# Performance work log

Measured on AMD Instinct MI355X. Metric: run time of the kernel, lower is better.

## Reference

```python
import jax, jax.numpy as jnp
import numpy as np

T, B, I, H = 512, 64, 1024, 1024
FORGET_BIAS = 1.0


def setup_inputs() -> dict:
    key = jax.random.key(0)
    ks = jax.random.split(key, 5)
    s = 0.02
    return {
        "x": jax.random.normal(ks[0], (T, B, I), dtype=jnp.float32),
        "Wx0": jax.random.normal(ks[1], (4 * H, I), dtype=jnp.float32) * s,
        "Wh0": jax.random.normal(ks[2], (4 * H, H), dtype=jnp.float32) * s,
        "Wx1": jax.random.normal(ks[3], (4 * H, H), dtype=jnp.float32) * s,
        "Wh1": jax.random.normal(ks[4], (4 * H, H), dtype=jnp.float32) * s,
    }


def _cell(x_t, h, c, Wx, Wh):
    # ifgo: [B, 4H]; gate chunk order in source is i, j, f, o
    ifgo = x_t @ Wx.T + h @ Wh.T
    i, j, f, o = jnp.split(ifgo, 4, axis=-1)
    c_next = c * jax.nn.sigmoid(f + FORGET_BIAS) + jax.nn.sigmoid(i) * jnp.tanh(j)
    h_next = jax.nn.sigmoid(o) * jnp.tanh(c_next)
    return h_next, c_next


def reference(x, Wx0, Wh0, Wx1, Wh1):
    b, hdim = x.shape[1], Wh0.shape[1]
    z = jnp.zeros((b, hdim), dtype=x.dtype)

    def step(carry, x_t):
        h0, c0, h1, c1 = carry
        h0, c0 = _cell(x_t, h0, c0, Wx0, Wh0)
        h1, c1 = _cell(h0, h1, c1, Wx1, Wh1)
        return (h0, c0, h1, c1), h1

    (h0, c0, h1, c1), out = jax.lax.scan(step, (z, z, z, z), x)
    h = jnp.stack([h0, h1])  # [n_layers, B, H]
    c = jnp.stack([c0, c1])
    return out, h, c
```

## Files before the change

### kernel.cpp

```cpp
#include <hip/hip_runtime.h>


#define T_STEPS 512
#define BATCH   64
#define HDIM    1024
#define KTOT    2048
#define BK      128
#define NITER   (KTOT / BK)
#define LDSTR   136
#define BH      (BATCH * HDIM)

typedef __bf16 bf16x8 __attribute__((ext_vector_type(8)));
typedef __bf16 bf16x4 __attribute__((ext_vector_type(4)));
typedef float  f32x4  __attribute__((ext_vector_type(4)));

__device__ __forceinline__ float sigm_(float x) { return 1.0f / (1.0f + __expf(-x)); }
__device__ __forceinline__ float tanh_(float x) {
    float e = __expf(-2.0f * fabsf(x));
    float t = (1.0f - e) / (1.0f + e);
    return copysignf(t, x);
}

__global__ __launch_bounds__(256) void lstm_step2(
    const __bf16* __restrict__ Ax0, const __bf16* __restrict__ Ah0,
    const __bf16* __restrict__ W0,  float* __restrict__ c0,
    __bf16* __restrict__ hb0, float* __restrict__ hf0, int en0,
    const __bf16* __restrict__ Ax1, const __bf16* __restrict__ Ah1,
    const __bf16* __restrict__ W1,  float* __restrict__ c1,
    __bf16* __restrict__ hb1, float* __restrict__ hf1, int en1)
{
    __shared__ __bf16 As[64 * LDSTR];
    __shared__ __bf16 Bs[64 * LDSTR];

    int bid = blockIdx.x;
    const __bf16 *Ax, *Ah, *W;
    float *c, *hf;
    __bf16 *hb;
    if (bid < 64) {
        if (!en0) return;
        Ax = Ax0; Ah = Ah0; W = W0; c = c0; hb = hb0; hf = hf0;
    } else {
        if (!en1) return;
        Ax = Ax1; Ah = Ah1; W = W1; c = c1; hb = hb1; hf = hf1; bid -= 64;
    }
    const int n0   = bid * 16;
    const int tid  = threadIdx.x;
    const int wave = tid >> 6;
    const int lane = tid & 63;
    const int sr   = tid >> 2;
    const int kc   = (tid & 3) * 32;
    const int wrow = (sr >> 4) * 1024 + n0 + (sr & 15);

    f32x4 acc[4] = {};

    bf16x8 pa[4], pb[4];
    {
        const __bf16* s = Ax + sr * 1024 + kc;
        #pragma unroll
        for (int u = 0; u < 4; ++u) pa[u] = *(const bf16x8*)(s + u * 8);
        const __bf16* w = W + wrow * 2048 + kc;
        #pragma unroll
        for (int u = 0; u < 4; ++u) pb[u] = *(const bf16x8*)(w + u * 8);
    }

    for (int it = 0; it < NITER; ++it) {
        #pragma unroll
        for (int u = 0; u < 4; ++u) *(bf16x8*)&As[sr * LDSTR + kc + u * 8] = pa[u];
        #pragma unroll
        for (int u = 0; u < 4; ++u) *(bf16x8*)&Bs[sr * LDSTR + kc + u * 8] = pb[u];
        __syncthreads();

        if (it + 1 < NITER) {
            int kb = (it + 1) * BK;
            const __bf16* s = (kb < 1024 ? Ax + sr * 1024 + kb
                                         : Ah + sr * 1024 + (kb - 1024)) + kc;
            #pragma unroll
            for (int u = 0; u < 4; ++u) pa[u] = *(const bf16x8*)(s + u * 8);
            const __bf16* w = W + wrow * 2048 + kb + kc;
            #pragma unroll
            for (int u = 0; u < 4; ++u) pb[u] = *(const bf16x8*)(w + u * 8);
        }

        const int lrow = lane & 15;
        const int lk   = (lane >> 4) * 8;
        #pragma unroll
        for (int s4 = 0; s4 < 4; ++s4) {
            bf16x8 af = *(bf16x8*)&As[(wave * 16 + lrow) * LDSTR + s4 * 32 + lk];
            #pragma unroll
            for (int g = 0; g < 4; ++g) {
                bf16x8 bf = *(bf16x8*)&Bs[(g * 16 + lrow) * LDSTR + s4 * 32 + lk];
                acc[g] = __builtin_amdgcn_mfma_f32_16x16x32_bf16(af, bf, acc[g], 0, 0, 0);
            }
        }
        __syncthreads();
    }

    const int n  = n0 + (lane & 15);
    const int mb = wave * 16 + (lane >> 4) * 4;
    #pragma unroll
    for (int r = 0; r < 4; ++r) {
        int m = mb + r;
        float gi = acc[0][r], gj = acc[1][r], gf = acc[2][r], go = acc[3][r];
        float cold = c[m * HDIM + n];
        float cn = cold * sigm_(gf + 1.0f) + sigm_(gi) * tanh_(gj);
        float hn = sigm_(go) * tanh_(cn);
        c[m * HDIM + n]  = cn;
        hb[m * HDIM + n] = (__bf16)hn;
        hf[m * HDIM + n] = hn;
    }
}

__global__ void convW(const float* __restrict__ Wx, const float* __restrict__ Wh,
                      __bf16* __restrict__ dst) {
    int i = blockIdx.x * 256 + threadIdx.x;
    int e = i * 4;
    int n = e >> 11;
    int k = e & 2047;
    const float* src = (k < 1024) ? (Wx + n * 1024 + k) : (Wh + n * 1024 + (k - 1024));
    float4 v = *(const float4*)src;
    bf16x4 o = { (__bf16)v.x, (__bf16)v.y, (__bf16)v.z, (__bf16)v.w };
    *(bf16x4*)(dst + e) = o;
}

__global__ void convX(const float* __restrict__ x, __bf16* __restrict__ dst) {
    int i = blockIdx.x * 256 + threadIdx.x;
    int e = i * 4;
    float4 v = *(const float4*)(x + e);
    bf16x4 o = { (__bf16)v.x, (__bf16)v.y, (__bf16)v.z, (__bf16)v.w };
    *(bf16x4*)(dst + e) = o;
}

__global__ void initz(__bf16* h0s, __bf16* h1s, float* c0, float* c1) {
    int i = blockIdx.x * 256 + threadIdx.x;
    h0s[i] = (__bf16)0.0f;
    h1s[i] = (__bf16)0.0f;
    c0[i] = 0.0f;
    c1[i] = 0.0f;
}

__global__ void epilogue_k(float* __restrict__ out, const float* __restrict__ h0f,
                           const float* __restrict__ c0, const float* __restrict__ c1) {
    int i = blockIdx.x * 256 + threadIdx.x;
    float* hout = out + (size_t)T_STEPS * BH;
    hout[i]      = h0f[i];
    hout[BH + i] = out[(size_t)(T_STEPS - 1) * BH + i];
    float* cout = hout + 2 * BH;
    cout[i]      = c0[i];
    cout[BH + i] = c1[i];
}

extern "C" void kernel_launch(void* const* d_in, const int* in_sizes, int n_in,
                              void* d_out, int out_size, void* d_ws, size_t ws_size,
                              hipStream_t stream) {
    const float* x   = (const float*)d_in[0];
    const float* Wx0 = (const float*)d_in[1];
    const float* Wh0 = (const float*)d_in[2];
    const float* Wx1 = (const float*)d_in[3];
    const float* Wh1 = (const float*)d_in[4];
    float* out = (float*)d_out;

    char* p = (char*)d_ws;
    __bf16* W0c = (__bf16*)p; p += (size_t)4096 * 2048 * 2;
    __bf16* W1c = (__bf16*)p; p += (size_t)4096 * 2048 * 2;
    __bf16* Xb  = (__bf16*)p; p += (size_t)T_STEPS * BH * 2;
    __bf16* h0s = (__bf16*)p; p += (size_t)2 * BH * 2;
    __bf16* h1s = (__bf16*)p; p += (size_t)2 * BH * 2;
    float*  c0v = (float*)p;  p += (size_t)BH * 4;
    float*  c1v = (float*)p;  p += (size_t)BH * 4;
    float*  h0f = (float*)p;  p += (size_t)BH * 4;

    convW<<<8192, 256, 0, stream>>>(Wx0, Wh0, W0c);
    convW<<<8192, 256, 0, stream>>>(Wx1, Wh1, W1c);
    convX<<<32768, 256, 0, stream>>>(x, Xb);
    initz<<<256, 256, 0, stream>>>(h0s, h1s, c0v, c1v);

    for (int s = 0; s <= T_STEPS; ++s) {
        int en0 = (s < T_STEPS);
        int en1 = (s >= 1);
        int t1  = en1 ? (s - 1) : 0;
        const __bf16* Ax0 = Xb + (size_t)(en0 ? s : 0) * BH;
        const __bf16* Ah0 = h0s + (size_t)(s & 1) * BH;
        __bf16*       hb0 = h0s + (size_t)((s & 1) ^ 1) * BH;
        const __bf16* Ax1 = h0s + (size_t)(s & 1) * BH;
        const __bf16* Ah1 = h1s + (size_t)(t1 & 1) * BH;
        __bf16*       hb1 = h1s + (size_t)((t1 & 1) ^ 1) * BH;
        float*        o1  = out + (size_t)t1 * BH;
        lstm_step2<<<128, 256, 0, stream>>>(Ax0, Ah0, W0c, c0v, hb0, h0f, en0,
                                            Ax1, Ah1, W1c, c1v, hb1, o1, en1);
    }

    epilogue_k<<<256, 256, 0, stream>>>(out, h0f, c0v, c1v);
}
```

Before: 10.50 ms.

## Replace per-step launches with persistent kernel holding weights in LDS

Measured after the change: 13.09 ms. 1.25x slower.

```diff
diff --git a/kernel.cpp b/kernel.cpp
--- a/kernel.cpp
+++ b/kernel.cpp
@@ -4,11 +4,8 @@
 #define T_STEPS 512
 #define BATCH   64
 #define HDIM    1024
-#define KTOT    2048
-#define BK      128
-#define NITER   (KTOT / BK)
-#define LDSTR   136
 #define BH      (BATCH * HDIM)
+#define LDS_BYTES (32 * 4096)
 
 typedef __bf16 bf16x8 __attribute__((ext_vector_type(8)));
 typedef __bf16 bf16x4 __attribute__((ext_vector_type(4)));
@@ -21,92 +18,127 @@
     return copysignf(t, x);
 }
 
-__global__ __launch_bounds__(256) void lstm_step2(
-    const __bf16* __restrict__ Ax0, const __bf16* __restrict__ Ah0,
-    const __bf16* __restrict__ W0,  float* __restrict__ c0,
-    __bf16* __restrict__ hb0, float* __restrict__ hf0, int en0,
-    const __bf16* __restrict__ Ax1, const __bf16* __restrict__ Ah1,
-    const __bf16* __restrict__ W1,  float* __restrict__ c1,
-    __bf16* __restrict__ hb1, float* __restrict__ hf1, int en1)
+__global__ __launch_bounds__(256, 1) void lstm_persist(
+    const __bf16* __restrict__ Xb,
+    const __bf16* __restrict__ W0, const __bf16* __restrict__ W1,
+    __bf16* __restrict__ h0s, __bf16* __restrict__ h1s,
+    float* __restrict__ out, float* __restrict__ h0f,
+    float* __restrict__ c0v, float* __restrict__ c1v,
+    int* __restrict__ flags)
 {
-    __shared__ __bf16 As[64 * LDSTR];
-    __shared__ __bf16 Bs[64 * LDSTR];
-
-    int bid = blockIdx.x;
-    const __bf16 *Ax, *Ah, *W;
-    float *c, *hf;
-    __bf16 *hb;
-    if (bid < 64) {
-        if (!en0) return;
-        Ax = Ax0; Ah = Ah0; W = W0; c = c0; hb = hb0; hf = hf0;
-    } else {
-        if (!en1) return;
-        Ax = Ax1; Ah = Ah1; W = W1; c = c1; hb = hb1; hf = hf1; bid -= 64;
+    extern __shared__ char smem[];
+    const int bid   = blockIdx.x;
+    const int tid   = threadIdx.x;
+    const int layer = bid >> 7;
+    const int cb    = bid & 127;
+    const int n0    = cb * 8;
+    const __bf16* W = layer ? W1 : W0;
+
+    for (int idx = tid; idx < 32 * 256; idx += 256) {
+        int lr = idx >> 8, ch = idx & 255;
+        int wrow = (lr >> 3) * 1024 + n0 + (lr & 7);
+        bf16x8 v = *(const bf16x8*)(W + (size_t)wrow * 2048 + ch * 8);
+        int db = lr * 4096 + ((ch * 16) ^ ((lr & 7) << 4));
+        *(bf16x8*)(smem + db) = v;
     }
-    const int n0   = bid * 16;
-    const int tid  = threadIdx.x;
+    __syncthreads();
+
+    const int lane = tid & 63;
     const int wave = tid >> 6;
-    const int lane = tid & 63;
-    const int sr   = tid >> 2;
-    const int kc   = (tid & 3) * 32;
-    const int wrow = (sr >> 4) * 1024 + n0 + (sr & 15);
-
-    f32x4 acc[4] = {};
-
-    bf16x8 pa[4], pb[4];
-    {
-        const __bf16* s = Ax + sr * 1024 + kc;
-        #pragma unroll
-        for (int u = 0; u < 4; ++u) pa[u] = *(const bf16x8*)(s + u * 8);
-        const __bf16* w = W + wrow * 2048 + kc;
-        #pragma unroll
-        for (int u = 0; u < 4; ++u) pb[u] = *(const bf16x8*)(w + u * 8);
-    }
-
-    for (int it = 0; it < NITER; ++it) {
-        #pragma unroll
-        for (int u = 0; u < 4; ++u) *(bf16x8*)&As[sr * LDSTR + kc + u * 8] = pa[u];
-        #pragma unroll
-        for (int u = 0; u < 4; ++u) *(bf16x8*)&Bs[sr * LDSTR + kc + u * 8] = pb[u];
-        __syncthreads();
-
-        if (it + 1 < NITER) {
-            int kb = (it + 1) * BK;
-            const __bf16* s = (kb < 1024 ? Ax + sr * 1024 + kb
-                                         : Ah + sr * 1024 + (kb - 1024)) + kc;
-            #pragma unroll
-            for (int u = 0; u < 4; ++u) pa[u] = *(const bf16x8*)(s + u * 8);
-            const __bf16* w = W + wrow * 2048 + kb + kc;
-            #pragma unroll
-            for (int u = 0; u < 4; ++u) pb[u] = *(const bf16x8*)(w + u * 8);
-        }
-
-        const int lrow = lane & 15;
-        const int lk   = (lane >> 4) * 8;
-        #pragma unroll
-        for (int s4 = 0; s4 < 4; ++s4) {
-            bf16x8 af = *(bf16x8*)&As[(wave * 16 + lrow) * LDSTR + s4 * 32 + lk];
-            #pragma unroll
-            for (int g = 0; g < 4; ++g) {
-                bf16x8 bf = *(bf16x8*)&Bs[(g * 16 + lrow) * LDSTR + s4 * 32 + lk];
-                acc[g] = __builtin_amdgcn_mfma_f32_16x16x32_bf16(af, bf, acc[g], 0, 0, 0);
+    const int arow = wave * 16 + (lane & 15);
+    const int kb   = (lane >> 4) * 8;
+    const int r0   = lane & 15;
+    const int r1   = 16 + r0;
+    const int lo16 = (kb * 2) ^ ((r0 & 3) << 4);
+    const int s6   = (r0 >> 2) & 1;
+    const char* pb0 = smem + r0 * 4096 + lo16;
+    const char* pb1 = smem + r1 * 4096 + lo16;
+    const char* pb0e = pb0 + s6 * 64;
+    const char* pb0o = pb0 - s6 * 64;
+    const char* pb1e = pb1 + s6 * 64;
+    const char* pb1o = pb1 - s6 * 64;
+
+    const int  lr   = lane & 15;
+    const bool lo   = lr < 8;
+    const int  col  = n0 + (lr & 7);
+    const int  mrow = wave * 16 + (lane >> 4) * 4;
+
+    float creg0 = 0.0f, creg1 = 0.0f;
+
+    for (int s = 0; s <= T_STEPS; ++s) {
+        const int en = layer ? (s >= 1) : (s < T_STEPS);
+        if (en) {
+            const int t = layer ? s - 1 : s;
+            const __bf16* Ax = layer ? (h0s + (size_t)(s & 1) * BH)
+                                     : (Xb  + (size_t)s * BH);
+            const __bf16* Ah = layer ? (h1s + (size_t)(t & 1) * BH)
+                                     : (h0s + (size_t)(s & 1) * BH);
+            __bf16* hb = layer ? (h1s + (size_t)((t & 1) ^ 1) * BH)
+                               : (h0s + (size_t)((s & 1) ^ 1) * BH);
+
+            const __bf16* ax = Ax + arow * 1024 + kb;
+            const __bf16* ah = Ah + arow * 1024 + kb;
+
+            f32x4 acc0 = {}, acc1 = {};
+            bf16x8 p[8];
+            #pragma unroll
+            for (int u = 0; u < 8; ++u) p[u] = *(const bf16x8*)(ax + u * 32);
+            #pragma unroll
+            for (int base = 0; base < 64; base += 8) {
+                #pragma unroll
+                for (int u = 0; u < 8; ++u) {
+                    const int ks = base + u;
+                    bf16x8 a = p[u];
+                    const int pf = ks + 8;
+                    if (pf < 32)      p[u] = *(const bf16x8*)(ax + pf * 32);
+                    else if (pf < 64) p[u] = *(const bf16x8*)(ah + (pf - 32) * 32);
+                    bf16x8 b0 = *(const bf16x8*)(((ks & 1) ? pb0o : pb0e) + ks * 64);
+                    bf16x8 b1 = *(const bf16x8*)(((ks & 1) ? pb1o : pb1e) + ks * 64);
+                    acc0 = __builtin_amdgcn_mfma_f32_16x16x32_bf16(a, b0, acc0, 0, 0, 0);
+                    acc1 = __builtin_amdgcn_mfma_f32_16x16x32_bf16(a, b1, acc1, 0, 0, 0);
+                }
+            }
+
+            float q0[4], q1[4];
+            #pragma unroll
+            for (int r2 = 0; r2 < 4; ++r2) {
+                q0[r2] = __shfl_xor(acc0[r2], 8, 64);
+                q1[r2] = __shfl_xor(acc1[r2], 8, 64);
+            }
+            const int rb = lo ? 0 : 2;
+            #pragma unroll
+            for (int rr = 0; rr < 2; ++rr) {
+                const int r2 = rb + rr;
+                float gi = lo ? acc0[r2] : q0[r2];
+                float gj = lo ? q0[r2]   : acc0[r2];
+                float gf = lo ? acc1[r2] : q1[r2];
+                float go = lo ? q1[r2]   : acc1[r2];
+                float cold = rr ? creg1 : creg0;
+                float cn = cold * sigm_(gf + 1.0f) + sigm_(gi) * tanh_(gj);
+                float hn = sigm_(go) * tanh_(cn);
+                if (rr) creg1 = cn; else creg0 = cn;
+                const int m = mrow + r2;
+                hb[m * HDIM + col] = (__bf16)hn;
+                if (layer) out[(size_t)t * BH + m * HDIM + col] = hn;
+                else if (s == T_STEPS - 1) h0f[m * HDIM + col] = hn;
+                if (t == T_STEPS - 1) (layer ? c1v : c0v)[m * HDIM + col] = cn;
             }
         }
-        __syncthreads();
-    }
-
-    const int n  = n0 + (lane & 15);
-    const int mb = wave * 16 + (lane >> 4) * 4;
-    #pragma unroll
-    for (int r = 0; r < 4; ++r) {
-        int m = mb + r;
-        float gi = acc[0][r], gj = acc[1][r], gf = acc[2][r], go = acc[3][r];
-        float cold = c[m * HDIM + n];
-        float cn = cold * sigm_(gf + 1.0f) + sigm_(gi) * tanh_(gj);
-        float hn = sigm_(go) * tanh_(cn);
-        c[m * HDIM + n]  = cn;
-        hb[m * HDIM + n] = (__bf16)hn;
-        hf[m * HDIM + n] = hn;
+
+        if (s < T_STEPS) {
+            __syncthreads();
+            if (tid == 0)
+                __hip_atomic_store(&flags[bid], s + 1, __ATOMIC_RELEASE,
+                                   __HIP_MEMORY_SCOPE_AGENT);
+            int ok;
+            do {
+                int v = __hip_atomic_load(&flags[tid], __ATOMIC_RELAXED,
+                                          __HIP_MEMORY_SCOPE_AGENT);
+                ok = __syncthreads_and(v >= s + 1);
+                if (!ok) __builtin_amdgcn_s_sleep(2);
+            } while (!ok);
+            __builtin_amdgcn_fence(__ATOMIC_ACQUIRE, "agent");
+        }
     }
 }
 
@@ -130,12 +162,15 @@
     *(bf16x4*)(dst + e) = o;
 }
 
-__global__ void initz(__bf16* h0s, __bf16* h1s, float* c0, float* c1) {
+__global__ void initz(__bf16* h0s, __bf16* h1s, float* c0, float* c1,
+                      float* h0f, int* flags) {
     int i = blockIdx.x * 256 + threadIdx.x;
     h0s[i] = (__bf16)0.0f;
     h1s[i] = (__bf16)0.0f;
     c0[i] = 0.0f;
     c1[i] = 0.0f;
+    h0f[i] = 0.0f;
+    if (i < 256) flags[i] = 0;
 }
 
 __global__ void epilogue_k(float* __restrict__ out, const float* __restrict__ h0f,
@@ -168,26 +203,18 @@
     float*  c0v = (float*)p;  p += (size_t)BH * 4;
     float*  c1v = (float*)p;  p += (size_t)BH * 4;
     float*  h0f = (float*)p;  p += (size_t)BH * 4;
+    int*  flags = (int*)p;    p += 256 * 4;
+
+    hipFuncSetAttribute(reinterpret_cast<const void*>(lstm_persist),
+                        hipFuncAttributeMaxDynamicSharedMemorySize, LDS_BYTES);
 
     convW<<<8192, 256, 0, stream>>>(Wx0, Wh0, W0c);
     convW<<<8192, 256, 0, stream>>>(Wx1, Wh1, W1c);
     convX<<<32768, 256, 0, stream>>>(x, Xb);
-    initz<<<256, 256, 0, stream>>>(h0s, h1s, c0v, c1v);
-
-    for (int s = 0; s <= T_STEPS; ++s) {
-        int en0 = (s < T_STEPS);
-        int en1 = (s >= 1);
-        int t1  = en1 ? (s - 1) : 0;
-        const __bf16* Ax0 = Xb + (size_t)(en0 ? s : 0) * BH;
-        const __bf16* Ah0 = h0s + (size_t)(s & 1) * BH;
-        __bf16*       hb0 = h0s + (size_t)((s & 1) ^ 1) * BH;
-        const __bf16* Ax1 = h0s + (size_t)(s & 1) * BH;
-        const __bf16* Ah1 = h1s + (size_t)(t1 & 1) * BH;
-        __bf16*       hb1 = h1s + (size_t)((t1 & 1) ^ 1) * BH;
-        float*        o1  = out + (size_t)t1 * BH;
-        lstm_step2<<<128, 256, 0, stream>>>(Ax0, Ah0, W0c, c0v, hb0, h0f, en0,
-                                            Ax1, Ah1, W1c, c1v, hb1, o1, en1);
-    }
+    initz<<<256, 256, 0, stream>>>(h0s, h1s, c0v, c1v, h0f, flags);
+
+    lstm_persist<<<256, 256, LDS_BYTES, stream>>>(Xb, W0c, W1c, h0s, h1s,
+                                                  out, h0f, c0v, c1v, flags);
 
     epilogue_k<<<256, 256, 0, stream>>>(out, h0f, c0v, c1v);
 }
```
